# Kernel optimization log

Hardware: AMD Instinct MI355X
Metric: run time of the kernel (lower is better)

The kernel has to match this reference:

```python
import jax, jax.numpy as jnp
import numpy as np

B, S, D, H = 2, 2048, 1024, 16
HD = D // H  # head_dim = 64
ROPE_BASE = 10000.0


def _rope_cos_sin(seq_len, head_dim, dtype):
    inv_freq = 1.0 / (ROPE_BASE ** (jnp.arange(0, head_dim, 2, dtype=jnp.float32) / head_dim))
    t = jnp.arange(seq_len, dtype=jnp.float32)
    freqs = jnp.einsum('i,j->ij', t, inv_freq)            # [S, HD/2]
    emb = jnp.concatenate([freqs, freqs], axis=-1)        # [S, HD]
    return jnp.cos(emb).astype(dtype), jnp.sin(emb).astype(dtype)


def _rotate_half(x):
    x1, x2 = jnp.split(x, 2, axis=-1)
    return jnp.concatenate([-x2, x1], axis=-1)


def setup_inputs() -> dict:
    key = jax.random.key(0)
    ks = jax.random.split(key, 5)
    scale = 1.0 / np.sqrt(D)
    x = jax.random.normal(ks[0], (B, S, D), dtype=jnp.float32)
    wq = jax.random.normal(ks[1], (D, D), dtype=jnp.float32) * scale
    wk = jax.random.normal(ks[2], (D, D), dtype=jnp.float32) * scale
    wv = jax.random.normal(ks[3], (D, D), dtype=jnp.float32) * scale
    wo = jax.random.normal(ks[4], (D, D), dtype=jnp.float32) * scale
    # causal additive mask: 0 on/below diagonal, -1e9 above
    causal = jnp.triu(jnp.full((S, S), -1e9, dtype=jnp.float32), k=1)
    attention_mask = causal[None, None, :, :]
    return {'x': x, 'attention_mask': attention_mask, 'wq': wq, 'wk': wk, 'wv': wv, 'wo': wo}


def reference(x, attention_mask, wq, wk, wv, wo):
    b, s, d = x.shape
    scale = 1.0 / np.sqrt(HD)
    # projections (torch Linear: y = x @ W.T)
    q = (x @ wq.T).reshape(b, s, H, HD).transpose(0, 2, 1, 3)  # [B,H,S,HD]
    k = (x @ wk.T).reshape(b, s, H, HD).transpose(0, 2, 1, 3)
    v = (x @ wv.T).reshape(b, s, H, HD).transpose(0, 2, 1, 3)
    cos, sin = _rope_cos_sin(s, HD, x.dtype)                   # [S, HD]
    cos = cos[None, None]
    sin = sin[None, None]
    q = q * cos + _rotate_half(q) * sin
    k = k * cos + _rotate_half(k) * sin
    scores = jnp.einsum('bhqd,bhkd->bhqk', q, k) * scale       # [B,H,S,S]
    scores = scores + attention_mask
    probs = jax.nn.softmax(scores, axis=-1)
    out = jnp.einsum('bhqk,bhkd->bhqd', probs, v)              # [B,H,S,HD]
    out = out.transpose(0, 2, 1, 3).reshape(b, s, d)
    return out @ wo.T
```

## Files before the change

### kernel.cpp

```cpp
#include <hip/hip_runtime.h>
#include <cstdint>
#include <cstddef>

typedef __attribute__((ext_vector_type(8))) _Float16 half8;
typedef __attribute__((ext_vector_type(4))) _Float16 half4;
typedef __attribute__((ext_vector_type(4))) float f32x4;

#define NB 2
#define NS 2048
#define ND 1024
#define NH 16
#define NHD 64
#define NM (NB * NS)

__device__ __forceinline__ void cvt8(const float* __restrict__ s,
                                     _Float16* __restrict__ d, int g) {
  const float4* s4 = (const float4*)s + (size_t)g * 2;
  float4 a = s4[0], b = s4[1];
  half8 h;
  h[0] = (_Float16)a.x; h[1] = (_Float16)a.y;
  h[2] = (_Float16)a.z; h[3] = (_Float16)a.w;
  h[4] = (_Float16)b.x; h[5] = (_Float16)b.y;
  h[6] = (_Float16)b.z; h[7] = (_Float16)b.w;
  *(half8*)(d + (size_t)g * 8) = h;
}

__global__ void prep(const float* __restrict__ x,
                     const float* __restrict__ wq, const float* __restrict__ wk,
                     const float* __restrict__ wv, const float* __restrict__ wo,
                     _Float16* __restrict__ xb,
                     _Float16* __restrict__ wqb, _Float16* __restrict__ wkb,
                     _Float16* __restrict__ wvb, _Float16* __restrict__ wob,
                     float* __restrict__ cosT, float* __restrict__ sinT) {
  int i = blockIdx.x * 256 + threadIdx.x;
  if (i < 524288) {
    cvt8(x, xb, i);
  } else if (i < 1048576) {
    int j = i - 524288;
    int k = j >> 17, g = j & 131071;
    const float* ws = (k == 0) ? wq : (k == 1) ? wk : (k == 2) ? wv : wo;
    _Float16* wd = (k == 0) ? wqb : (k == 1) ? wkb : (k == 2) ? wvb : wob;
    cvt8(ws, wd, g);
  } else if (i < 1056768) {
    int t0 = (i - 1048576) * 8;
#pragma unroll
    for (int e = 0; e < 8; ++e) {
      int t = t0 + e;
      int s = t >> 5, j = t & 31;
      float inv = expf(-(float)(2 * j) * (9.210340371976184f / 64.0f));
      float ang = (float)s * inv;
      cosT[t] = cosf(ang);
      sinT[t] = sinf(ang);
    }
  }
}

__device__ __forceinline__ void gload_lds16(const void* g, void* lds) {
  __builtin_amdgcn_global_load_lds(
      (const __attribute__((address_space(1))) unsigned int*)g,
      (__attribute__((address_space(3))) unsigned int*)lds, 16, 0, 0);
}

__device__ __forceinline__ float exp2_fast(float x) {
  float r;
  asm("v_exp_f32 %0, %1" : "=v"(r) : "v"(x));
  return r;
}

__device__ __forceinline__ void gemm_mainloop(const _Float16* __restrict__ A,
                                              const _Float16* __restrict__ Bw,
                                              _Float16* As, _Float16* Bs,
                                              int brow, int bcol,
                                              int lane, int wid,
                                              f32x4 acc[4][4]) {
  const int l15 = lane & 15, l4 = lane >> 4;
  const int wr = wid >> 1, wc = wid & 1;
  const int srow = lane >> 2, scol = (lane & 3) * 8;
  const _Float16* Ab = A + (size_t)(brow + srow) * ND + scol;
  const _Float16* Bb = Bw + (size_t)(bcol + srow) * ND + scol;

  for (int kt = 0; kt < ND / 32; ++kt) {
    const int k0 = kt * 32;
#pragma unroll
    for (int c = 0; c < 2; ++c) {
      const int chunk = wid * 2 + c;
      gload_lds16(Ab + (size_t)chunk * 16 * ND + k0, As + chunk * 512);
      gload_lds16(Bb + (size_t)chunk * 16 * ND + k0, Bs + chunk * 512);
    }
    __syncthreads();
    half8 af[4], bf[4];
#pragma unroll
    for (int m = 0; m < 4; ++m)
      af[m] = *(const half8*)(As + (wr * 64 + m * 16 + l15) * 32 + l4 * 8);
#pragma unroll
    for (int n = 0; n < 4; ++n)
      bf[n] = *(const half8*)(Bs + (wc * 64 + n * 16 + l15) * 32 + l4 * 8);
#pragma unroll
    for (int m = 0; m < 4; ++m)
#pragma unroll
      for (int n = 0; n < 4; ++n)
        acc[m][n] = __builtin_amdgcn_mfma_f32_16x16x32_f16(af[m], bf[n],
                                                           acc[m][n], 0, 0, 0);
    __syncthreads();
  }
}

__launch_bounds__(256, 2)
__global__ void qkv_gemm(const _Float16* __restrict__ X,
                         const _Float16* __restrict__ Wq,
                         const _Float16* __restrict__ Wk,
                         const _Float16* __restrict__ Wv,
                         _Float16* __restrict__ Qb,
                         _Float16* __restrict__ Kb,
                         _Float16* __restrict__ Vt,
                         const float* __restrict__ cosT,
                         const float* __restrict__ sinT) {
  __shared__ __align__(16) _Float16 As[128 * 32];
  __shared__ __align__(16) _Float16 Bs[128 * 32];
  const int tid = threadIdx.x, lane = tid & 63, wid = tid >> 6;
  const int l15 = lane & 15, l4 = lane >> 4;
  const int wr = wid >> 1, wc = wid & 1;
  const int brow = blockIdx.y * 128, bcol = blockIdx.x * 128;
  const int mode = blockIdx.z;
  const _Float16* W = (mode == 0) ? Wq : (mode == 1 ? Wk : Wv);

  f32x4 acc[4][4] = {};
  gemm_mainloop(X, W, As, Bs, brow, bcol, lane, wid, acc);

  const int b = brow >> 11;
  const int sbase = (brow & (NS - 1)) + wr * 64;
  const int h = (bcol >> 6) + wc;

  if (mode < 2) {
    _Float16* oh = ((mode == 0) ? Qb : Kb) + (size_t)(b * NH + h) * NS * NHD;
#pragma unroll
    for (int m = 0; m < 4; ++m) {
#pragma unroll
      for (int r = 0; r < 4; ++r) {
        const int s = sbase + m * 16 + l4 * 4 + r;
#pragma unroll
        for (int n = 0; n < 2; ++n) {
          const int hd = n * 16 + l15;
          const float c = cosT[s * 32 + hd];
          const float sn = sinT[s * 32 + hd];
          const float lo = acc[m][n][r], hi = acc[m][n + 2][r];
          oh[(size_t)s * NHD + hd]      = (_Float16)(lo * c - hi * sn);
          oh[(size_t)s * NHD + hd + 32] = (_Float16)(hi * c + lo * sn);
        }
      }
    }
  } else {
#pragma unroll
    for (int m = 0; m < 4; ++m) {
      const int s0 = sbase + m * 16 + l4 * 4;
#pragma unroll
      for (int n = 0; n < 4; ++n) {
        const int hd = n * 16 + l15;
        half4 pk;
        pk[0] = (_Float16)acc[m][n][0];
        pk[1] = (_Float16)acc[m][n][1];
        pk[2] = (_Float16)acc[m][n][2];
        pk[3] = (_Float16)acc[m][n][3];
        *(half4*)(Vt + ((size_t)(b * NH + h) * NHD + hd) * NS + s0) = pk;
      }
    }
  }
}

__launch_bounds__(256, 4)
__global__ void flash_attn(const _Float16* __restrict__ Qb,
                           const _Float16* __restrict__ Kb,
                           const _Float16* __restrict__ Vt,
                           _Float16* __restrict__ Ob) {
  __shared__ __align__(16) _Float16 Ks[2][64 * 64];
  __shared__ __align__(16) _Float16 Vs[2][64 * 64];
  const int tid = threadIdx.x, lane = tid & 63, wid = tid >> 6;
  const int l15 = lane & 15, l4 = lane >> 4;
  const int bh = blockIdx.x & 31, pr = blockIdx.x >> 5;
  const _Float16* Qh = Qb + (size_t)bh * NS * NHD;
  const char* Kg = (const char*)(Kb + (size_t)bh * NS * NHD);
  const char* Vg = (const char*)(Vt + (size_t)bh * NHD * NS);

  const float K1 = 0.125f * 1.4426950408889634f;
  const int swz_lane = ((lane >> 3) & 7) << 4;
  const int qloc = wid * 16 + l15;
  const int rswz = (l15 & 7) << 4;
  const int b = bh >> 4, h = bh & 15;

  for (int item = 0; item < 2; ++item) {
    const int qt = item ? pr : 31 - pr;

    half8 qf[2];
#pragma unroll
    for (int kk = 0; kk < 2; ++kk)
      qf[kk] = *(const half8*)&Qh[(size_t)(qt * 64 + wid * 16 + l15) * NHD + kk * 32 + l4 * 8];

    f32x4 oacc[4] = {};
    float mrun = -3.0e38f, lrun = 0.f;
    const int nkt = qt + 1;

#pragma unroll
    for (int c = 0; c < 2; ++c) {
      const int chunk = wid * 2 + c;
      const int slot = chunk * 1024 + lane * 16;
      const int sw = slot ^ swz_lane;
      gload_lds16(Kg + sw, (char*)&Ks[0][0] + slot);
      const int vrow = slot >> 7;
      gload_lds16(Vg + (size_t)vrow * (NS * 2) + (sw & 127), (char*)&Vs[0][0] + slot);
    }
    __syncthreads();

    int cur = 0;
    for (int kt = 0; kt < nkt; ++kt) {
      if (kt + 1 < nkt) {
        const size_t knext = (size_t)(kt + 1);
#pragma unroll
        for (int c = 0; c < 2; ++c) {
          const int chunk = wid * 2 + c;
          const int slot = chunk * 1024 + lane * 16;
          const int sw = slot ^ swz_lane;
          gload_lds16(Kg + knext * 8192 + sw, (char*)&Ks[cur ^ 1][0] + slot);
          const int vrow = slot >> 7;
          gload_lds16(Vg + (size_t)vrow * (NS * 2) + knext * 128 + (sw & 127),
                      (char*)&Vs[cur ^ 1][0] + slot);
        }
      }

      const bool diag = (kt == qt);
      const char* Kbuf = (const char*)&Ks[cur][0];
      const char* Vbuf = (const char*)&Vs[cur][0];

      f32x4 sacc[4] = {};
      __builtin_amdgcn_s_setprio(1);
#pragma unroll
      for (int kk = 0; kk < 2; ++kk) {
#pragma unroll
        for (int n = 0; n < 4; ++n) {
          if (diag && n > wid) continue;
          const int off = ((n * 16 + l15) * 128 + kk * 64 + l4 * 16) ^ rswz;
          half8 kf = *(const half8*)(Kbuf + off);
          sacc[n] = __builtin_amdgcn_mfma_f32_16x16x32_f16(kf, qf[kk], sacc[n], 0, 0, 0);
        }
      }
      __builtin_amdgcn_s_setprio(0);

      float t[16];
#pragma unroll
      for (int n = 0; n < 4; ++n)
#pragma unroll
        for (int r = 0; r < 4; ++r) {
          float v = sacc[n][r] * K1;
          if (diag) {
            const int ki = n * 16 + l4 * 4 + r;
            v = (ki > qloc) ? -3.0e38f : v;
          }
          t[n * 4 + r] = v;
        }
      float mx = t[0];
#pragma unroll
      for (int j = 1; j < 16; ++j) mx = fmaxf(mx, t[j]);
      mx = fmaxf(mx, __shfl_xor(mx, 16, 64));
      mx = fmaxf(mx, __shfl_xor(mx, 32, 64));
      const float mnew = fmaxf(mrun, mx);
      const float alpha = exp2_fast(mrun - mnew);
      mrun = mnew;
      float ps[16], rs = 0.f;
#pragma unroll
      for (int j = 0; j < 16; ++j) {
        ps[j] = exp2_fast(t[j] - mnew);
        rs += ps[j];
      }
      rs += __shfl_xor(rs, 16, 64);
      rs += __shfl_xor(rs, 32, 64);
      lrun = lrun * alpha + rs;
#pragma unroll
      for (int n = 0; n < 4; ++n) {
        oacc[n][0] *= alpha; oacc[n][1] *= alpha;
        oacc[n][2] *= alpha; oacc[n][3] *= alpha;
      }

      __builtin_amdgcn_s_setprio(1);
#pragma unroll
      for (int c = 0; c < 2; ++c) {
        if (diag && c == 1 && wid < 2) continue;
        half8 pb;
#pragma unroll
        for (int j = 0; j < 8; ++j)
          pb[j] = (_Float16)ps[(2 * c + (j >> 2)) * 4 + (j & 3)];
#pragma unroll
        for (int n = 0; n < 4; ++n) {
          const int off0 = ((n * 16 + l15) * 128 + c * 64 + l4 * 8) ^ rswz;
          const int off1 = off0 ^ 32;
          half4 vlo = *(const half4*)(Vbuf + off0);
          half4 vhi = *(const half4*)(Vbuf + off1);
          half8 va;
          va[0] = vlo[0]; va[1] = vlo[1]; va[2] = vlo[2]; va[3] = vlo[3];
          va[4] = vhi[0]; va[5] = vhi[1]; va[6] = vhi[2]; va[7] = vhi[3];
          oacc[n] = __builtin_amdgcn_mfma_f32_16x16x32_f16(va, pb, oacc[n], 0, 0, 0);
        }
      }
      __builtin_amdgcn_s_setprio(0);

      __syncthreads();
      cur ^= 1;
    }

    const int s = qt * 64 + wid * 16 + l15;
    const float invl = 1.0f / lrun;
#pragma unroll
    for (int n = 0; n < 4; ++n) {
      half4 o;
      o[0] = (_Float16)(oacc[n][0] * invl);
      o[1] = (_Float16)(oacc[n][1] * invl);
      o[2] = (_Float16)(oacc[n][2] * invl);
      o[3] = (_Float16)(oacc[n][3] * invl);
      *(half4*)&Ob[((size_t)(b * NS + s)) * ND + h * NHD + n * 16 + l4 * 4] = o;
    }
  }
}

__launch_bounds__(256, 2)
__global__ void proj_gemm(const _Float16* __restrict__ A,
                          const _Float16* __restrict__ W,
                          float* __restrict__ out) {
  __shared__ __align__(16) _Float16 As[128 * 32];
  __shared__ __align__(16) _Float16 Bs[128 * 32];
  const int tid = threadIdx.x, lane = tid & 63, wid = tid >> 6;
  const int l15 = lane & 15, l4 = lane >> 4;
  const int wr = wid >> 1, wc = wid & 1;
  const int brow = blockIdx.y * 128, bcol = blockIdx.x * 128;
  f32x4 acc[4][4] = {};
  gemm_mainloop(A, W, As, Bs, brow, bcol, lane, wid, acc);
#pragma unroll
  for (int m = 0; m < 4; ++m)
#pragma unroll
    for (int n = 0; n < 4; ++n)
#pragma unroll
      for (int r = 0; r < 4; ++r)
        out[(size_t)(brow + wr * 64 + m * 16 + l4 * 4 + r) * ND
            + bcol + wc * 64 + n * 16 + l15] = acc[m][n][r];
}

extern "C" void kernel_launch(void* const* d_in, const int* in_sizes, int n_in,
                              void* d_out, int out_size, void* d_ws, size_t ws_size,
                              hipStream_t stream) {
  const float* x  = (const float*)d_in[0];
  const float* wq = (const float*)d_in[2];
  const float* wk = (const float*)d_in[3];
  const float* wv = (const float*)d_in[4];
  const float* wo = (const float*)d_in[5];
  float* out = (float*)d_out;

  char* w = (char*)d_ws;
  _Float16* xb   = (_Float16*)(w);
  _Float16* wqb  = (_Float16*)(w + (8ull  << 20));
  _Float16* wkb  = (_Float16*)(w + (10ull << 20));
  _Float16* wvb  = (_Float16*)(w + (12ull << 20));
  _Float16* wob  = (_Float16*)(w + (14ull << 20));
  _Float16* Qb   = (_Float16*)(w + (16ull << 20));
  _Float16* Kb   = (_Float16*)(w + (24ull << 20));
  _Float16* Vt   = (_Float16*)(w + (32ull << 20));
  _Float16* Ob   = (_Float16*)(w + (40ull << 20));
  float*    cosT = (float*)   (w + (48ull << 20));
  float*    sinT = (float*)   (w + (48ull << 20) + (1ull << 18));

  dim3 blk(256);
  prep<<<4128, blk, 0, stream>>>(x, wq, wk, wv, wo, xb, wqb, wkb, wvb, wob,
                                 cosT, sinT);
  qkv_gemm<<<dim3(8, 32, 3), blk, 0, stream>>>(xb, wqb, wkb, wvb, Qb, Kb, Vt,
                                               cosT, sinT);
  flash_attn<<<512, blk, 0, stream>>>(Qb, Kb, Vt, Ob);
  proj_gemm<<<dim3(8, 32), blk, 0, stream>>>(Ob, wob, out);
}
```

Baseline: 109.5 us.

## Drop LDS staging in flash attention, load K/V directly into registers

The flash attention kernel stops staging K and V tiles through double-buffered shared memory with async global-to-LDS copies and barriers. Each wave now loads its K and V fragments straight from global memory into registers. Blocks shrink to two waves, with twice as many blocks, so each block covers half of a 64-row query tile. This removes LDS traffic and __syncthreads. In exchange, every wave re-reads the same K/V tile from global memory or cache, which raises L2 traffic and exposes load latency because there is no prefetch.

Result: slower. 245.0 us (+123.7%).

```diff
diff --git a/kernel.cpp b/kernel.cpp
--- a/kernel.cpp
+++ b/kernel.cpp
@@ -167,25 +167,24 @@
   }
 }
 
-__launch_bounds__(256, 4)
+__launch_bounds__(128, 2)
 __global__ void flash_attn(const _Float16* __restrict__ Qb,
                            const _Float16* __restrict__ Kb,
                            const _Float16* __restrict__ Vt,
                            _Float16* __restrict__ Ob) {
-  __shared__ __align__(16) _Float16 Ks[2][64 * 64];
-  __shared__ __align__(16) _Float16 Vs[2][64 * 64];
   const int tid = threadIdx.x, lane = tid & 63, wid = tid >> 6;
   const int l15 = lane & 15, l4 = lane >> 4;
-  const int bh = blockIdx.x & 31, pr = blockIdx.x >> 5;
+  const int bh = blockIdx.x & 31;
+  const int ph = blockIdx.x >> 5;
+  const int pr = ph >> 1, h = ph & 1;
+  const int ws = h * 2 + wid;
   const _Float16* Qh = Qb + (size_t)bh * NS * NHD;
-  const char* Kg = (const char*)(Kb + (size_t)bh * NS * NHD);
-  const char* Vg = (const char*)(Vt + (size_t)bh * NHD * NS);
+  const _Float16* Kh = Kb + (size_t)bh * NS * NHD;
+  const _Float16* Vh = Vt + (size_t)bh * NHD * NS;
 
   const float K1 = 0.125f * 1.4426950408889634f;
-  const int swz_lane = ((lane >> 3) & 7) << 4;
-  const int qloc = wid * 16 + l15;
-  const int rswz = (l15 & 7) << 4;
-  const int b = bh >> 4, h = bh & 15;
+  const int qloc = ws * 16 + l15;
+  const int b = bh >> 4, hh = bh & 15;
 
   for (int item = 0; item < 2; ++item) {
     const int qt = item ? pr : 31 - pr;
@@ -193,42 +192,26 @@
     half8 qf[2];
 #pragma unroll
     for (int kk = 0; kk < 2; ++kk)
-      qf[kk] = *(const half8*)&Qh[(size_t)(qt * 64 + wid * 16 + l15) * NHD + kk * 32 + l4 * 8];
+      qf[kk] = *(const half8*)&Qh[(size_t)(qt * 64 + ws * 16 + l15) * NHD + kk * 32 + l4 * 8];
 
     f32x4 oacc[4] = {};
     float mrun = -3.0e38f, lrun = 0.f;
-    const int nkt = qt + 1;
-
-#pragma unroll
-    for (int c = 0; c < 2; ++c) {
-      const int chunk = wid * 2 + c;
-      const int slot = chunk * 1024 + lane * 16;
-      const int sw = slot ^ swz_lane;
-      gload_lds16(Kg + sw, (char*)&Ks[0][0] + slot);
-      const int vrow = slot >> 7;
-      gload_lds16(Vg + (size_t)vrow * (NS * 2) + (sw & 127), (char*)&Vs[0][0] + slot);
-    }
-    __syncthreads();
-
-    int cur = 0;
-    for (int kt = 0; kt < nkt; ++kt) {
-      if (kt + 1 < nkt) {
-        const size_t knext = (size_t)(kt + 1);
-#pragma unroll
-        for (int c = 0; c < 2; ++c) {
-          const int chunk = wid * 2 + c;
-          const int slot = chunk * 1024 + lane * 16;
-          const int sw = slot ^ swz_lane;
-          gload_lds16(Kg + knext * 8192 + sw, (char*)&Ks[cur ^ 1][0] + slot);
-          const int vrow = slot >> 7;
-          gload_lds16(Vg + (size_t)vrow * (NS * 2) + knext * 128 + (sw & 127),
-                      (char*)&Vs[cur ^ 1][0] + slot);
-        }
-      }
-
+
+    const _Float16* kp = Kh + (size_t)l15 * NHD + l4 * 8;
+    const _Float16* vp = Vh + (size_t)l15 * NS + l4 * 4;
+
+    for (int kt = 0; kt <= qt; ++kt) {
       const bool diag = (kt == qt);
-      const char* Kbuf = (const char*)&Ks[cur][0];
-      const char* Vbuf = (const char*)&Vs[cur][0];
+      const _Float16* kpt = kp + (size_t)kt * 64 * NHD;
+      const _Float16* vpt = vp + (size_t)kt * 64;
+
+      half8 kf[2][4];
+#pragma unroll
+      for (int n = 0; n < 4; ++n) {
+#pragma unroll
+        for (int kk = 0; kk < 2; ++kk)
+          kf[kk][n] = *(const half8*)(kpt + n * 16 * NHD + kk * 32);
+      }
 
       f32x4 sacc[4] = {};
       __builtin_amdgcn_s_setprio(1);
@@ -236,13 +219,21 @@
       for (int kk = 0; kk < 2; ++kk) {
 #pragma unroll
         for (int n = 0; n < 4; ++n) {
-          if (diag && n > wid) continue;
-          const int off = ((n * 16 + l15) * 128 + kk * 64 + l4 * 16) ^ rswz;
-          half8 kf = *(const half8*)(Kbuf + off);
-          sacc[n] = __builtin_amdgcn_mfma_f32_16x16x32_f16(kf, qf[kk], sacc[n], 0, 0, 0);
+          if (diag && n > ws) continue;
+          sacc[n] = __builtin_amdgcn_mfma_f32_16x16x32_f16(kf[kk][n], qf[kk], sacc[n], 0, 0, 0);
         }
       }
       __builtin_amdgcn_s_setprio(0);
+
+      half4 vlo[2][4], vhi[2][4];
+#pragma unroll
+      for (int c = 0; c < 2; ++c) {
+#pragma unroll
+        for (int n = 0; n < 4; ++n) {
+          vlo[c][n] = *(const half4*)(vpt + n * 16 * NS + c * 32);
+          vhi[c][n] = *(const half4*)(vpt + n * 16 * NS + c * 32 + 16);
+        }
+      }
 
       float t[16];
 #pragma unroll
@@ -282,30 +273,25 @@
       __builtin_amdgcn_s_setprio(1);
 #pragma unroll
       for (int c = 0; c < 2; ++c) {
-        if (diag && c == 1 && wid < 2) continue;
+        if (diag && c == 1 && ws < 2) continue;
         half8 pb;
 #pragma unroll
         for (int j = 0; j < 8; ++j)
           pb[j] = (_Float16)ps[(2 * c + (j >> 2)) * 4 + (j & 3)];
 #pragma unroll
         for (int n = 0; n < 4; ++n) {
-          const int off0 = ((n * 16 + l15) * 128 + c * 64 + l4 * 8) ^ rswz;
-          const int off1 = off0 ^ 32;
-          half4 vlo = *(const half4*)(Vbuf + off0);
-          half4 vhi = *(const half4*)(Vbuf + off1);
           half8 va;
-          va[0] = vlo[0]; va[1] = vlo[1]; va[2] = vlo[2]; va[3] = vlo[3];
-          va[4] = vhi[0]; va[5] = vhi[1]; va[6] = vhi[2]; va[7] = vhi[3];
+          va[0] = vlo[c][n][0]; va[1] = vlo[c][n][1];
+          va[2] = vlo[c][n][2]; va[3] = vlo[c][n][3];
+          va[4] = vhi[c][n][0]; va[5] = vhi[c][n][1];
+          va[6] = vhi[c][n][2]; va[7] = vhi[c][n][3];
           oacc[n] = __builtin_amdgcn_mfma_f32_16x16x32_f16(va, pb, oacc[n], 0, 0, 0);
         }
       }
       __builtin_amdgcn_s_setprio(0);
-
-      __syncthreads();
-      cur ^= 1;
-    }
-
-    const int s = qt * 64 + wid * 16 + l15;
+    }
+
+    const int s = qt * 64 + ws * 16 + l15;
     const float invl = 1.0f / lrun;
 #pragma unroll
     for (int n = 0; n < 4; ++n) {
@@ -314,7 +300,7 @@
       o[1] = (_Float16)(oacc[n][1] * invl);
       o[2] = (_Float16)(oacc[n][2] * invl);
       o[3] = (_Float16)(oacc[n][3] * invl);
-      *(half4*)&Ob[((size_t)(b * NS + s)) * ND + h * NHD + n * 16 + l4 * 4] = o;
+      *(half4*)&Ob[((size_t)(b * NS + s)) * ND + hh * NHD + n * 16 + l4 * 4] = o;
     }
   }
 }
@@ -369,6 +355,6 @@
                                  cosT, sinT);
   qkv_gemm<<<dim3(8, 32, 3), blk, 0, stream>>>(xb, wqb, wkb, wvb, Qb, Kb, Vt,
                                                cosT, sinT);
-  flash_attn<<<512, blk, 0, stream>>>(Qb, Kb, Vt, Ob);
+  flash_attn<<<1024, dim3(128), 0, stream>>>(Qb, Kb, Vt, Ob);
   proj_gemm<<<dim3(8, 32), blk, 0, stream>>>(Ob, wob, out);
 }
```

## Deepen flash-attention K/V prefetch to two tiles ahead with four LDS buffers

Applied to the files above, without the earlier changes.

Replaces the double-buffered K/V LDS staging with a four-slot ring that prefetches tile kt+2 while computing tile kt. Explicit vmcnt waits allow one tile's loads to stay in flight across the barrier, so global latency is hidden over two iterations. LDS usage doubles to 64KB per block and launch bounds drop from 4 to 2 blocks per CU, which cuts occupancy. Correctness relies on the manual vmcnt counts matching the four async loads issued per stage.

Result: no change. 110.8 us (+1.1%).

```diff
diff --git a/kernel.cpp b/kernel.cpp
--- a/kernel.cpp
+++ b/kernel.cpp
@@ -167,13 +167,13 @@
   }
 }
 
-__launch_bounds__(256, 4)
+__launch_bounds__(256, 2)
 __global__ void flash_attn(const _Float16* __restrict__ Qb,
                            const _Float16* __restrict__ Kb,
                            const _Float16* __restrict__ Vt,
                            _Float16* __restrict__ Ob) {
-  __shared__ __align__(16) _Float16 Ks[2][64 * 64];
-  __shared__ __align__(16) _Float16 Vs[2][64 * 64];
+  __shared__ __align__(16) _Float16 Ks[4][64 * 64];
+  __shared__ __align__(16) _Float16 Vs[4][64 * 64];
   const int tid = threadIdx.x, lane = tid & 63, wid = tid >> 6;
   const int l15 = lane & 15, l4 = lane >> 4;
   const int bh = blockIdx.x & 31, pr = blockIdx.x >> 5;
@@ -187,48 +187,47 @@
   const int rswz = (l15 & 7) << 4;
   const int b = bh >> 4, h = bh & 15;
 
-  for (int item = 0; item < 2; ++item) {
-    const int qt = item ? pr : 31 - pr;
-
-    half8 qf[2];
-#pragma unroll
-    for (int kk = 0; kk < 2; ++kk)
-      qf[kk] = *(const half8*)&Qh[(size_t)(qt * 64 + wid * 16 + l15) * NHD + kk * 32 + l4 * 8];
-
-    f32x4 oacc[4] = {};
-    float mrun = -3.0e38f, lrun = 0.f;
-    const int nkt = qt + 1;
-
+  auto stage = [&](int kt, int si) {
 #pragma unroll
     for (int c = 0; c < 2; ++c) {
       const int chunk = wid * 2 + c;
       const int slot = chunk * 1024 + lane * 16;
       const int sw = slot ^ swz_lane;
-      gload_lds16(Kg + sw, (char*)&Ks[0][0] + slot);
+      gload_lds16(Kg + (size_t)kt * 8192 + sw, (char*)&Ks[si][0] + slot);
       const int vrow = slot >> 7;
-      gload_lds16(Vg + (size_t)vrow * (NS * 2) + (sw & 127), (char*)&Vs[0][0] + slot);
-    }
-    __syncthreads();
-
-    int cur = 0;
+      gload_lds16(Vg + (size_t)vrow * (NS * 2) + kt * 128 + (sw & 127),
+                  (char*)&Vs[si][0] + slot);
+    }
+  };
+
+  for (int item = 0; item < 2; ++item) {
+    const int qt = item ? pr : 31 - pr;
+    const int nkt = qt + 1;
+
+    half8 qf[2];
+#pragma unroll
+    for (int kk = 0; kk < 2; ++kk)
+      qf[kk] = *(const half8*)&Qh[(size_t)(qt * 64 + wid * 16 + l15) * NHD + kk * 32 + l4 * 8];
+
+    f32x4 oacc[4] = {};
+    float mrun = -3.0e38f, lrun = 0.f;
+
+    stage(0, 0);
+    if (nkt > 1) {
+      stage(1, 1);
+      asm volatile("s_waitcnt vmcnt(4)" ::: "memory");
+    } else {
+      asm volatile("s_waitcnt vmcnt(0)" ::: "memory");
+    }
+    __builtin_amdgcn_s_barrier();
+    __builtin_amdgcn_sched_barrier(0);
+
     for (int kt = 0; kt < nkt; ++kt) {
-      if (kt + 1 < nkt) {
-        const size_t knext = (size_t)(kt + 1);
-#pragma unroll
-        for (int c = 0; c < 2; ++c) {
-          const int chunk = wid * 2 + c;
-          const int slot = chunk * 1024 + lane * 16;
-          const int sw = slot ^ swz_lane;
-          gload_lds16(Kg + knext * 8192 + sw, (char*)&Ks[cur ^ 1][0] + slot);
-          const int vrow = slot >> 7;
-          gload_lds16(Vg + (size_t)vrow * (NS * 2) + knext * 128 + (sw & 127),
-                      (char*)&Vs[cur ^ 1][0] + slot);
-        }
-      }
+      if (kt + 2 < nkt) stage(kt + 2, (kt + 2) & 3);
 
       const bool diag = (kt == qt);
-      const char* Kbuf = (const char*)&Ks[cur][0];
-      const char* Vbuf = (const char*)&Vs[cur][0];
+      const char* Kbuf = (const char*)&Ks[kt & 3][0];
+      const char* Vbuf = (const char*)&Vs[kt & 3][0];
 
       f32x4 sacc[4] = {};
       __builtin_amdgcn_s_setprio(1);
@@ -301,8 +300,10 @@
       }
       __builtin_amdgcn_s_setprio(0);
 
-      __syncthreads();
-      cur ^= 1;
+      if (kt + 2 < nkt) asm volatile("s_waitcnt vmcnt(4)" ::: "memory");
+      else              asm volatile("s_waitcnt vmcnt(0)" ::: "memory");
+      __builtin_amdgcn_s_barrier();
+      __builtin_amdgcn_sched_barrier(0);
     }
 
     const int s = qt * 64 + wid * 16 + l15;
```
